# Kernel tuning notes

Hardware: AMD Instinct MI355X
Metric: run time of the kernel (lower is better)

## Reference

```python
import jax, jax.numpy as jnp
import numpy as np

N, E, F = 32768, 524288, 16          # nodes, edges, num_filters
S_IN, V_IN = 64, 32                  # input irreps: 64x0e + 32x1o  (dim 64 + 96 = 160)
NRBF = 32                            # radial basis size of f_ij
LN2 = float(np.log(2.0))

def ssp(x):
    # shifted softplus, the standard SchNet activation
    return jax.nn.softplus(x) - LN2

def setup_inputs() -> dict:
    key = jax.random.key(0)
    ks = jax.random.split(key, 16)
    x = jax.random.normal(ks[0], (N, S_IN + 3 * V_IN), jnp.float32)
    idx_i = jax.random.randint(ks[1], (E,), 0, N)
    idx_j = jax.random.randint(ks[2], (E,), 0, N)
    f_ij = jax.random.normal(ks[3], (E, NRBF), jnp.float32)
    rcut_ij = jax.random.uniform(ks[4], (E,), jnp.float32)
    Yr_ij = jax.random.normal(ks[5], (E, 4), jnp.float32)  # 1x0e + 1x1o
    # equivariant Linear 1: (64x0e+32x1o) -> num_filters*(1x0e+1x1o) = 16x0e+16x1o
    W1_0e = jax.random.normal(ks[6], (S_IN, F), jnp.float32)
    W1_1o = jax.random.normal(ks[7], (V_IN, F), jnp.float32)
    # filter MLP: NRBF -> F -> num_irreps(6*F)
    mW1 = jax.random.normal(ks[8], (NRBF, F), jnp.float32) / np.sqrt(NRBF)
    mb1 = jnp.zeros((F,), jnp.float32)
    mW2 = jax.random.normal(ks[9], (F, 6 * F), jnp.float32) / np.sqrt(F)
    mb2 = jnp.zeros((6 * F,), jnp.float32)
    # equivariant Linear 2: (2Fx0e+2Fx1o+Fx1e+Fx2e) -> input irreps (1e/2e paths drop)
    W2_0e = jax.random.normal(ks[10], (2 * F, S_IN), jnp.float32)
    W2_1o = jax.random.normal(ks[11], (2 * F, V_IN), jnp.float32)
    # equivariant Linear 3: input irreps -> input irreps
    W3_0e = jax.random.normal(ks[12], (S_IN, S_IN), jnp.float32)
    W3_1o = jax.random.normal(ks[13], (V_IN, V_IN), jnp.float32)
    return dict(x=x, f_ij=f_ij, rcut_ij=rcut_ij, Yr_ij=Yr_ij,
                W1_0e=W1_0e, W1_1o=W1_1o, mW1=mW1, mb1=mb1, mW2=mW2, mb2=mb2,
                W2_0e=W2_0e, W2_1o=W2_1o, W3_0e=W3_0e, W3_1o=W3_1o,
                idx_i=idx_i, idx_j=idx_j)

def reference(x, f_ij, rcut_ij, Yr_ij, W1_0e, W1_1o, mW1, mb1, mW2, mb2,
              W2_0e, W2_1o, W3_0e, W3_1o, idx_i, idx_j):
    n = x.shape[0]
    s = x[:, :S_IN]                                  # [N, 64]  0e channels
    v = x[:, S_IN:].reshape(n, V_IN, 3)              # [N, 32, 3] 1o channels
    # Linear 1 (per-irrep channel mixing, e3nn fan-in normalization)
    s1 = (s @ W1_0e) / np.sqrt(S_IN)                 # [N, F]
    v1 = jnp.einsum('ncd,cf->nfd', v, W1_1o) / np.sqrt(V_IN)  # [N, F, 3]
    # gather neighbor features (x_j = x[idx_j], mul_to_axis -> per-filter irreps)
    sj = s1[idx_j]                                   # [E, F]
    vj = v1[idx_j]                                   # [E, F, 3]
    y0 = Yr_ij[:, 0]                                 # [E]
    y1 = Yr_ij[:, 1:4]                               # [E, 3]
    # tensor product (0e+1o) x (0e+1o) -> 2x0e + 2x1o + 1x1e + 1x2e, per filter
    o0a = sj * y0[:, None]                                            # 0e: 0e x 0e
    o0b = jnp.einsum('efd,ed->ef', vj, y1) / np.sqrt(3.0)             # 0e: 1o.1o
    o1a = sj[:, :, None] * y1[:, None, :]                             # 1o: 0e x 1o
    o1b = vj * y0[:, None, None]                                      # 1o: 1o x 0e
    o1e = jnp.cross(vj, y1[:, None, :]) / np.sqrt(2.0)                # 1e: 1o ^ 1o
    ux, uy, uz = vj[..., 0], vj[..., 1], vj[..., 2]
    wx, wy, wz = y1[:, None, 0], y1[:, None, 1], y1[:, None, 2]
    o2 = jnp.stack([(ux * wy + uy * wx) / np.sqrt(2.0),
                    (uy * wz + uz * wy) / np.sqrt(2.0),
                    (2.0 * uz * wz - ux * wx - uy * wy) / np.sqrt(6.0),
                    (ux * wz + uz * wx) / np.sqrt(2.0),
                    (ux * wx - uy * wy) / np.sqrt(2.0)], axis=-1)      # 2e [E, F, 5]
    # filter MLP on radial features, gated by cutoff; one scalar per irrep
    W = ssp(f_ij @ mW1 + mb1) @ mW2 + mb2            # [E, 6F]
    W = W * rcut_ij[:, None]
    w0a, w0b, w1a, w1b, w1e, w2 = (W[:, k * F:(k + 1) * F] for k in range(6))
    seg = lambda z: jax.ops.segment_sum(z, idx_i, num_segments=N)
    # modulate + scatter-sum into center atoms
    n0a = seg(o0a * w0a); n0b = seg(o0b * w0b)                          # [N, F]
    n1a = seg(o1a * w1a[:, :, None]); n1b = seg(o1b * w1b[:, :, None])  # [N, F, 3]
    n1e = seg(o1e * w1e[:, :, None])                                    # [N, F, 3] (dropped by Linear 2)
    n2 = seg(o2 * w2[:, :, None])                                       # [N, F, 5] (dropped by Linear 2)
    n0 = jnp.concatenate([n0a, n0b], axis=-1)        # [N, 2F] 0e
    n1 = jnp.concatenate([n1a, n1b], axis=1)         # [N, 2F, 3] 1o
    del n1e, n2  # no matching output irrep in input_irreps -> e3nn Linear drops them
    # Linear 2 back to input irreps
    s2 = (n0 @ W2_0e) / np.sqrt(2 * F)               # [N, 64]
    v2 = jnp.einsum('nfd,fc->ncd', n1, W2_1o) / np.sqrt(2 * F)  # [N, 32, 3]
    # scalar activation on l=0 only
    s2 = ssp(s2)
    # Linear 3
    s3 = (s2 @ W3_0e) / np.sqrt(S_IN)
    v3 = jnp.einsum('ncd,ce->ned', v2, W3_1o) / np.sqrt(V_IN)
    return jnp.concatenate([s3, v3.reshape(n, -1)], axis=-1)  # [N, 160]
```

## Files before the change

### kernel.cpp

```cpp
#include <hip/hip_runtime.h>
#include <math.h>

#define NN 32768
#define NE 524288
#define RSTR 32
#define SREC_STR 36

__device__ __forceinline__ float sspf(float x) {
    const float INVLN2 = 1.4426950408889634f;
    const float LN2    = 0.69314718055994530942f;
    float t = __builtin_amdgcn_exp2f(-fabsf(x) * INVLN2);
    return fmaxf(x, 0.0f) + LN2 * __builtin_amdgcn_logf(1.0f + t) - LN2;
}

__global__ __launch_bounds__(256) void hist_kernel(
    const int* __restrict__ idx_i, int* __restrict__ counts, int* __restrict__ rank)
{
    int e = blockIdx.x * 256 + threadIdx.x;
    rank[e] = atomicAdd(&counts[idx_i[e]], 1);
}

__global__ __launch_bounds__(1024) void scan_kernel(
    const int* __restrict__ counts, int* __restrict__ start, int* __restrict__ order)
{
    __shared__ int tmp[1024];
    __shared__ int bins[64];
    __shared__ int bcur[64];
    int tid = threadIdx.x;
    int base = tid * 32;
    int cnt[32];
    int local[32];
    int sum = 0;
    const int4* c4 = (const int4*)(counts + base);
#pragma unroll
    for (int q = 0; q < 8; q++) {
        int4 v = c4[q];
        cnt[q*4+0] = v.x; cnt[q*4+1] = v.y; cnt[q*4+2] = v.z; cnt[q*4+3] = v.w;
        local[q*4+0] = sum; sum += v.x;
        local[q*4+1] = sum; sum += v.y;
        local[q*4+2] = sum; sum += v.z;
        local[q*4+3] = sum; sum += v.w;
    }
    tmp[tid] = sum;
    __syncthreads();
    for (int off = 1; off < 1024; off <<= 1) {
        int v = 0;
        if (tid >= off) v = tmp[tid - off];
        __syncthreads();
        if (tid >= off) tmp[tid] += v;
        __syncthreads();
    }
    int excl = tmp[tid] - sum;
#pragma unroll
    for (int k = 0; k < 32; k++) {
        start[base + k] = excl + local[k];
    }
    if (tid == 1023) start[NN] = tmp[1023];

    if (tid < 64) bins[tid] = 0;
    __syncthreads();
#pragma unroll
    for (int k = 0; k < 32; k++) {
        int d = cnt[k] > 63 ? 63 : cnt[k];
        atomicAdd(&bins[63 - d], 1);
    }
    __syncthreads();
    if (tid == 0) {
        int run = 0;
        for (int b = 0; b < 64; b++) { int c = bins[b]; bcur[b] = run; run += c; }
    }
    __syncthreads();
#pragma unroll
    for (int k = 0; k < 32; k++) {
        int d = cnt[k] > 63 ? 63 : cnt[k];
        int pos = atomicAdd(&bcur[63 - d], 1);
        order[pos] = base + k;
    }
}

__global__ __launch_bounds__(256) void pack_kernel(
    const float* __restrict__ f_ij,
    const float* __restrict__ rcut_ij,
    const float* __restrict__ Yr,
    const int*   __restrict__ idx_i,
    const int*   __restrict__ idx_j,
    const float* __restrict__ mW1,
    const float* __restrict__ mb1,
    const int*   __restrict__ start,
    const int*   __restrict__ rank,
    float* __restrict__ epack)
{
    __shared__ float sW1[512];
    __shared__ float sb1[16];
    __shared__ float srec[128 * SREC_STR];
    __shared__ int   sslot[128];
    int t = threadIdx.x;
    for (int k = t; k < 512; k += 256) sW1[k] = mW1[k];
    if (t < 16) sb1[t] = mb1[t];
    __syncthreads();

    int e = blockIdx.x * 256 + t;
    float h[16];
#pragma unroll
    for (int f = 0; f < 16; f++) h[f] = sb1[f];
    const float4* frow = (const float4*)(f_ij + (size_t)e * 32);
#pragma unroll
    for (int rq = 0; rq < 8; rq++) {
        float4 fv = frow[rq];
        int r = rq * 4;
#pragma unroll
        for (int f = 0; f < 16; f++)
            h[f] += fv.x * sW1[(r+0)*16+f] + fv.y * sW1[(r+1)*16+f]
                  + fv.z * sW1[(r+2)*16+f] + fv.w * sW1[(r+3)*16+f];
    }
    float rc = rcut_ij[e];
#pragma unroll
    for (int f = 0; f < 16; f++) h[f] = sspf(h[f]) * rc;

    int i = idx_i[e];
    int j = idx_j[e];
    float4 y = ((const float4*)Yr)[e];
    int slot = start[i] + rank[e];

#pragma unroll 1
    for (int p = 0; p < 2; p++) {
        if ((t >> 7) == p) {
            int r = t & 127;
            float* rp = srec + r * SREC_STR;
            float4* rp4 = (float4*)rp;
#pragma unroll
            for (int q = 0; q < 4; q++) rp4[q] = ((float4*)h)[q];
            rp4[4] = y;
            float4 tail; tail.x = rc; tail.y = __int_as_float(j);
            tail.z = 0.f; tail.w = 0.f;
            rp4[5] = tail;
            float4 z; z.x = 0.f; z.y = 0.f; z.z = 0.f; z.w = 0.f;
            rp4[6] = z;
            rp4[7] = z;
            sslot[r] = slot;
        }
        __syncthreads();
#pragma unroll
        for (int g = 0; g < 4; g++) {
            int idx = g * 256 + t;
            int r = idx >> 3;
            int qi = idx & 7;
            int s = sslot[r];
            float4 v = ((const float4*)(srec + r * SREC_STR))[qi];
            ((float4*)(epack + (size_t)s * RSTR))[qi] = v;
        }
        __syncthreads();
    }
}

__global__ __launch_bounds__(256) void embed_kernel(
    const float* __restrict__ x,
    const float* __restrict__ W1s,
    const float* __restrict__ W1v,
    float* __restrict__ embed)
{
    __shared__ float sWs[1024];
    __shared__ float sWv[512];
    int t = threadIdx.x;
    for (int k = t; k < 1024; k += 256) sWs[k] = W1s[k];
    for (int k = t; k < 512;  k += 256) sWv[k] = W1v[k];
    __syncthreads();

    int n = blockIdx.x * 256 + t;
    const float* xr = x + (size_t)n * 160;

    float s1[16];
#pragma unroll
    for (int f = 0; f < 16; f++) s1[f] = 0.f;
#pragma unroll 1
    for (int cc = 0; cc < 4; cc++) {
        float4 sv[4];
#pragma unroll
        for (int q = 0; q < 4; q++) sv[q] = ((const float4*)xr)[cc*4 + q];
#pragma unroll
        for (int q = 0; q < 4; q++) {
            int c = (cc*4 + q) * 4;
#pragma unroll
            for (int f = 0; f < 16; f++) {
                s1[f] += sv[q].x * sWs[(c+0)*16+f] + sv[q].y * sWs[(c+1)*16+f]
                       + sv[q].z * sWs[(c+2)*16+f] + sv[q].w * sWs[(c+3)*16+f];
            }
        }
    }

    float v1[48];
#pragma unroll
    for (int k = 0; k < 48; k++) v1[k] = 0.f;
#pragma unroll 1
    for (int cc = 0; cc < 4; cc++) {
        float4 vv[6];
#pragma unroll
        for (int q = 0; q < 6; q++) vv[q] = ((const float4*)(xr + 64))[cc*6 + q];
#pragma unroll
        for (int q = 0; q < 6; q++) {
            float vals[4] = {vv[q].x, vv[q].y, vv[q].z, vv[q].w};
#pragma unroll
            for (int u = 0; u < 4; u++) {
                int ml = q * 4 + u;
                int c = cc * 8 + ml / 3;
                int d = ml % 3;
                float val = vals[u];
#pragma unroll
                for (int f = 0; f < 16; f++)
                    v1[f*3+d] += val * sWv[c*16+f];
            }
        }
    }

    float ob[64];
    const float is32 = 0.17677669529663688f;
#pragma unroll
    for (int f = 0; f < 16; f++) {
        ob[f*4+0] = s1[f] * 0.125f;
        ob[f*4+1] = v1[f*3+0] * is32;
        ob[f*4+2] = v1[f*3+1] * is32;
        ob[f*4+3] = v1[f*3+2] * is32;
    }

    float4* eo = (float4*)(embed + (size_t)n * 64);
#pragma unroll
    for (int q = 0; q < 16; q++) eo[q] = ((float4*)ob)[q];
}

__global__ __launch_bounds__(256, 4) void nodeagg_kernel(
    const float* __restrict__ embed,
    const float* __restrict__ epack,
    const int*   __restrict__ start,
    const int*   __restrict__ order,
    const float* __restrict__ mW2,
    const float* __restrict__ mb2,
    float* __restrict__ acc)
{
    int t = threadIdx.x;
    int gid = blockIdx.x * 256 + t;
    int node = order[gid >> 4];
    int f = gid & 15;

    float wga[16], wgb[16], wgc[16], wgd[16];
#pragma unroll
    for (int k = 0; k < 16; k++) {
        wga[k] = mW2[k*96 + f];
        wgb[k] = mW2[k*96 + 16 + f];
        wgc[k] = mW2[k*96 + 32 + f];
        wgd[k] = mW2[k*96 + 48 + f];
    }
    float b0a = mb2[f], b0b = mb2[16+f], b1a = mb2[32+f], b1b = mb2[48+f];

    float aa = 0.f, ab = 0.f;
    float A1a0 = 0.f, A1a1 = 0.f, A1a2 = 0.f;
    float A1b0 = 0.f, A1b1 = 0.f, A1b2 = 0.f;

    int s0 = start[node];
    int s1 = start[node+1];

    for (int q = s0; q < s1; q++) {
        const float4* r4 = (const float4*)(epack + (size_t)q * RSTR);
        float4 h0 = r4[0], h1 = r4[1], h2 = r4[2], h3 = r4[3];
        float4 y  = r4[4], tl = r4[5];
        int j = __float_as_int(tl.y);
        float4 e4 = ((const float4*)(embed + (size_t)j * 64))[f];
        float rc = tl.x;

        float w0a = rc*b0a, w0b = rc*b0b, w1a = rc*b1a, w1b = rc*b1b;
        w0a += h0.x*wga[0]  + h0.y*wga[1]  + h0.z*wga[2]  + h0.w*wga[3]
             + h1.x*wga[4]  + h1.y*wga[5]  + h1.z*wga[6]  + h1.w*wga[7]
             + h2.x*wga[8]  + h2.y*wga[9]  + h2.z*wga[10] + h2.w*wga[11]
             + h3.x*wga[12] + h3.y*wga[13] + h3.z*wga[14] + h3.w*wga[15];
        w0b += h0.x*wgb[0]  + h0.y*wgb[1]  + h0.z*wgb[2]  + h0.w*wgb[3]
             + h1.x*wgb[4]  + h1.y*wgb[5]  + h1.z*wgb[6]  + h1.w*wgb[7]
             + h2.x*wgb[8]  + h2.y*wgb[9]  + h2.z*wgb[10] + h2.w*wgb[11]
             + h3.x*wgb[12] + h3.y*wgb[13] + h3.z*wgb[14] + h3.w*wgb[15];
        w1a += h0.x*wgc[0]  + h0.y*wgc[1]  + h0.z*wgc[2]  + h0.w*wgc[3]
             + h1.x*wgc[4]  + h1.y*wgc[5]  + h1.z*wgc[6]  + h1.w*wgc[7]
             + h2.x*wgc[8]  + h2.y*wgc[9]  + h2.z*wgc[10] + h2.w*wgc[11]
             + h3.x*wgc[12] + h3.y*wgc[13] + h3.z*wgc[14] + h3.w*wgc[15];
        w1b += h0.x*wgd[0]  + h0.y*wgd[1]  + h0.z*wgd[2]  + h0.w*wgd[3]
             + h1.x*wgd[4]  + h1.y*wgd[5]  + h1.z*wgd[6]  + h1.w*wgd[7]
             + h2.x*wgd[8]  + h2.y*wgd[9]  + h2.z*wgd[10] + h2.w*wgd[11]
             + h3.x*wgd[12] + h3.y*wgd[13] + h3.z*wgd[14] + h3.w*wgd[15];

        float sj = e4.x, vx = e4.y, vy = e4.z, vz = e4.w;
        aa += sj * y.x * w0a;
        ab += (vx*y.y + vy*y.z + vz*y.w) * w0b;
        float sw = sj * w1a;
        A1a0 += sw * y.y;
        A1a1 += sw * y.z;
        A1a2 += sw * y.w;
        float yw = y.x * w1b;
        A1b0 += vx * yw;
        A1b1 += vy * yw;
        A1b2 += vz * yw;
    }

    const float is3 = 0.5773502691896258f;
    float* o = acc + (size_t)node * 128;
    o[f]       = aa;
    o[16 + f]  = ab * is3;
    o[32 + f]  = A1a0;
    o[48 + f]  = A1a1;
    o[64 + f]  = A1a2;
    o[80 + f]  = A1b0;
    o[96 + f]  = A1b1;
    o[112 + f] = A1b2;
}


template<int LEN>
__device__ __forceinline__ void v2_seg(const float* a, int d, int cb,
    const float* __restrict__ W2v, float* V2, int ln)
{
    cb = __builtin_amdgcn_readfirstlane(cb);
    d  = __builtin_amdgcn_readfirstlane(d);
    const float is32 = 0.17677669529663688f;
    float na[16], nb[16];
    const float4* pa = (const float4*)(a + 32 + 16*d);
    const float4* pb = (const float4*)(a + 80 + 16*d);
#pragma unroll
    for (int q = 0; q < 4; q++) { ((float4*)na)[q] = pa[q]; ((float4*)nb)[q] = pb[q]; }
    float tacc[LEN];
#pragma unroll
    for (int c = 0; c < LEN; c++) tacc[c] = 0.f;
#pragma unroll
    for (int f = 0; f < 16; f++) {
        float fa = na[f], fb = nb[f];
#pragma unroll
        for (int c = 0; c < LEN; c++)
            tacc[c] += fa * W2v[f*32 + cb + c] + fb * W2v[(16+f)*32 + cb + c];
    }
    float* row = V2 + (d*64 + ln) * 33 + cb;
#pragma unroll
    for (int c = 0; c < LEN; c++) row[c] = tacc[c] * is32;
}

template<int LEN>
__device__ __forceinline__ void v3_seg(float* o, int d, int cb,
    const float* __restrict__ W3v, const float* V2, int ln)
{
    cb = __builtin_amdgcn_readfirstlane(cb);
    d  = __builtin_amdgcn_readfirstlane(d);
    const float is32 = 0.17677669529663688f;
    float tacc[LEN];
#pragma unroll
    for (int c = 0; c < LEN; c++) tacc[c] = 0.f;
    const float* row = V2 + (d*64 + ln) * 33;
#pragma unroll
    for (int k = 0; k < 32; k++) {
        float vk = row[k];
#pragma unroll
        for (int c = 0; c < LEN; c++) tacc[c] += vk * W3v[k*32 + cb + c];
    }
#pragma unroll
    for (int c = 0; c < LEN; c++) o[64 + (cb+c)*3 + d] = tacc[c] * is32;
}

__global__ __launch_bounds__(512, 4) void out_kernel(
    const float* __restrict__ acc,
    const float* __restrict__ W2s,
    const float* __restrict__ W2v,
    const float* __restrict__ W3s,
    const float* __restrict__ W3v,
    float* __restrict__ out)
{
    __shared__ float S2[64*65];
    __shared__ float V2[3*64*33];
    int t = threadIdx.x;
    int w = t >> 6, ln = t & 63;
    int node = blockIdx.x * 64 + ln;
    const float* a = acc + (size_t)node * 128;
    float* o = out + (size_t)node * 160;
    const float is32 = 0.17677669529663688f;

    if (w < 4) {
        int cb = __builtin_amdgcn_readfirstlane(w * 16);
        float n0r[32];
#pragma unroll
        for (int q = 0; q < 8; q++) ((float4*)n0r)[q] = ((const float4*)a)[q];
        float tacc[16];
#pragma unroll
        for (int c = 0; c < 16; c++) tacc[c] = 0.f;
#pragma unroll
        for (int k = 0; k < 32; k++) {
            float nk = n0r[k];
#pragma unroll
            for (int c = 0; c < 16; c++) tacc[c] += nk * W2s[k*64 + cb + c];
        }
        float* row = S2 + ln*65 + cb;
#pragma unroll
        for (int c = 0; c < 16; c++) row[c] = sspf(tacc[c] * is32);
    } else if (w == 4) {
        v2_seg<24>(a, 0, 0,  W2v, V2, ln);
    } else if (w == 5) {
        v2_seg<8> (a, 0, 24, W2v, V2, ln);
        v2_seg<16>(a, 1, 0,  W2v, V2, ln);
    } else if (w == 6) {
        v2_seg<16>(a, 1, 16, W2v, V2, ln);
        v2_seg<8> (a, 2, 0,  W2v, V2, ln);
    } else {
        v2_seg<24>(a, 2, 8,  W2v, V2, ln);
    }
    __syncthreads();
    if (w < 4) {
        int cb = __builtin_amdgcn_readfirstlane(w * 16);
        float tacc[16];
#pragma unroll
        for (int c = 0; c < 16; c++) tacc[c] = 0.f;
        const float* row = S2 + ln*65;
#pragma unroll
        for (int k = 0; k < 64; k++) {
            float sk = row[k];
#pragma unroll
            for (int c = 0; c < 16; c++) tacc[c] += sk * W3s[k*64 + cb + c];
        }
#pragma unroll
        for (int q = 0; q < 4; q++) {
            float4 r = {tacc[q*4+0]*0.125f, tacc[q*4+1]*0.125f,
                        tacc[q*4+2]*0.125f, tacc[q*4+3]*0.125f};
            ((float4*)(o + cb))[q] = r;
        }
    } else if (w == 4) {
        v3_seg<24>(o, 0, 0,  W3v, V2, ln);
    } else if (w == 5) {
        v3_seg<8> (o, 0, 24, W3v, V2, ln);
        v3_seg<16>(o, 1, 0,  W3v, V2, ln);
    } else if (w == 6) {
        v3_seg<16>(o, 1, 16, W3v, V2, ln);
        v3_seg<8> (o, 2, 0,  W3v, V2, ln);
    } else {
        v3_seg<24>(o, 2, 8,  W3v, V2, ln);
    }
}

extern "C" void kernel_launch(void* const* d_in, const int* in_sizes, int n_in,
                              void* d_out, int out_size, void* d_ws, size_t ws_size,
                              hipStream_t stream) {
    const float* x     = (const float*)d_in[0];
    const float* f_ij  = (const float*)d_in[1];
    const float* rcut  = (const float*)d_in[2];
    const float* Yr    = (const float*)d_in[3];
    const float* W1s   = (const float*)d_in[4];
    const float* W1v   = (const float*)d_in[5];
    const float* mW1   = (const float*)d_in[6];
    const float* mb1   = (const float*)d_in[7];
    const float* mW2   = (const float*)d_in[8];
    const float* mb2   = (const float*)d_in[9];
    const float* W2s   = (const float*)d_in[10];
    const float* W2v   = (const float*)d_in[11];
    const float* W3s   = (const float*)d_in[12];
    const float* W3v   = (const float*)d_in[13];
    const int*   idx_i = (const int*)d_in[14];
    const int*   idx_j = (const int*)d_in[15];
    float* out = (float*)d_out;

    float* fws   = (float*)d_ws;
    float* embed = fws;
    float* acc   = embed + (size_t)NN * 64;
    float* epack = acc   + (size_t)NN * 128;
    int* ibase   = (int*)(epack + (size_t)NE * RSTR);
    int* counts  = ibase;
    int* start   = counts + NN;
    int* rank    = start + NN + 1;
    int* order   = rank + NE;

    hipMemsetAsync(counts, 0, (size_t)NN * sizeof(int), stream);
    hist_kernel<<<NE/256, 256, 0, stream>>>(idx_i, counts, rank);
    scan_kernel<<<1, 1024, 0, stream>>>(counts, start, order);
    pack_kernel<<<NE/256, 256, 0, stream>>>(f_ij, rcut, Yr, idx_i, idx_j,
                                            mW1, mb1, start, rank, epack);
    embed_kernel<<<NN/256, 256, 0, stream>>>(x, W1s, W1v, embed);
    nodeagg_kernel<<<(NN*16)/256, 256, 0, stream>>>(embed, epack, start, order,
                                                    mW2, mb2, acc);
    out_kernel<<<NN/64, 512, 0, stream>>>(acc, W2s, W2v, W3s, W3v, out);
}
```

Before: 320.7 us.

## Write edge records in edge order and gather via permutation index in aggregation

The pack kernel now writes each edge's 128-byte record contiguously at its own edge index instead of scattering it to the sorted slot through a shared-memory staging pass. A new small kernel builds an edge permutation array, and the node aggregation kernel reads records indirectly through it. This trades coalesced scattered writes plus two block barriers for an extra index load and a non-contiguous gather of records per node in the aggregation loop.

```diff
diff --git a/kernel.cpp b/kernel.cpp
--- a/kernel.cpp
+++ b/kernel.cpp
@@ -4,7 +4,6 @@
 #define NN 32768
 #define NE 524288
 #define RSTR 32
-#define SREC_STR 36
 
 __device__ __forceinline__ float sspf(float x) {
     const float INVLN2 = 1.4426950408889634f;
@@ -78,22 +77,25 @@
     }
 }
 
+__global__ __launch_bounds__(256) void eorder_kernel(
+    const int* __restrict__ idx_i, const int* __restrict__ start,
+    const int* __restrict__ rank, int* __restrict__ eorder)
+{
+    int e = blockIdx.x * 256 + threadIdx.x;
+    eorder[start[idx_i[e]] + rank[e]] = e;
+}
+
 __global__ __launch_bounds__(256) void pack_kernel(
     const float* __restrict__ f_ij,
     const float* __restrict__ rcut_ij,
     const float* __restrict__ Yr,
-    const int*   __restrict__ idx_i,
     const int*   __restrict__ idx_j,
     const float* __restrict__ mW1,
     const float* __restrict__ mb1,
-    const int*   __restrict__ start,
-    const int*   __restrict__ rank,
     float* __restrict__ epack)
 {
     __shared__ float sW1[512];
     __shared__ float sb1[16];
-    __shared__ float srec[128 * SREC_STR];
-    __shared__ int   sslot[128];
     int t = threadIdx.x;
     for (int k = t; k < 512; k += 256) sW1[k] = mW1[k];
     if (t < 16) sb1[t] = mb1[t];
@@ -117,40 +119,19 @@
 #pragma unroll
     for (int f = 0; f < 16; f++) h[f] = sspf(h[f]) * rc;
 
-    int i = idx_i[e];
     int j = idx_j[e];
     float4 y = ((const float4*)Yr)[e];
-    int slot = start[i] + rank[e];
-
-#pragma unroll 1
-    for (int p = 0; p < 2; p++) {
-        if ((t >> 7) == p) {
-            int r = t & 127;
-            float* rp = srec + r * SREC_STR;
-            float4* rp4 = (float4*)rp;
-#pragma unroll
-            for (int q = 0; q < 4; q++) rp4[q] = ((float4*)h)[q];
-            rp4[4] = y;
-            float4 tail; tail.x = rc; tail.y = __int_as_float(j);
-            tail.z = 0.f; tail.w = 0.f;
-            rp4[5] = tail;
-            float4 z; z.x = 0.f; z.y = 0.f; z.z = 0.f; z.w = 0.f;
-            rp4[6] = z;
-            rp4[7] = z;
-            sslot[r] = slot;
-        }
-        __syncthreads();
-#pragma unroll
-        for (int g = 0; g < 4; g++) {
-            int idx = g * 256 + t;
-            int r = idx >> 3;
-            int qi = idx & 7;
-            int s = sslot[r];
-            float4 v = ((const float4*)(srec + r * SREC_STR))[qi];
-            ((float4*)(epack + (size_t)s * RSTR))[qi] = v;
-        }
-        __syncthreads();
-    }
+
+    float* rec = epack + (size_t)e * RSTR;
+    float4* r4 = (float4*)rec;
+#pragma unroll
+    for (int q = 0; q < 4; q++) r4[q] = ((float4*)h)[q];
+    r4[4] = y;
+    float4 tail; tail.x = rc; tail.y = __int_as_float(j); tail.z = 0.f; tail.w = 0.f;
+    r4[5] = tail;
+    float4 z; z.x = 0.f; z.y = 0.f; z.z = 0.f; z.w = 0.f;
+    r4[6] = z;
+    r4[7] = z;
 }
 
 __global__ __launch_bounds__(256) void embed_kernel(
@@ -232,6 +213,7 @@
     const float* __restrict__ epack,
     const int*   __restrict__ start,
     const int*   __restrict__ order,
+    const int*   __restrict__ eorder,
     const float* __restrict__ mW2,
     const float* __restrict__ mb2,
     float* __restrict__ acc)
@@ -259,7 +241,8 @@
     int s1 = start[node+1];
 
     for (int q = s0; q < s1; q++) {
-        const float4* r4 = (const float4*)(epack + (size_t)q * RSTR);
+        int e = eorder[q];
+        const float4* r4 = (const float4*)(epack + (size_t)e * RSTR);
         float4 h0 = r4[0], h1 = r4[1], h2 = r4[2], h3 = r4[3];
         float4 y  = r4[4], tl = r4[5];
         int j = __float_as_int(tl.y);
@@ -465,14 +448,16 @@
     int* start   = counts + NN;
     int* rank    = start + NN + 1;
     int* order   = rank + NE;
+    int* eorder  = order + NN;
 
     hipMemsetAsync(counts, 0, (size_t)NN * sizeof(int), stream);
     hist_kernel<<<NE/256, 256, 0, stream>>>(idx_i, counts, rank);
     scan_kernel<<<1, 1024, 0, stream>>>(counts, start, order);
-    pack_kernel<<<NE/256, 256, 0, stream>>>(f_ij, rcut, Yr, idx_i, idx_j,
-                                            mW1, mb1, start, rank, epack);
+    eorder_kernel<<<NE/256, 256, 0, stream>>>(idx_i, start, rank, eorder);
+    pack_kernel<<<NE/256, 256, 0, stream>>>(f_ij, rcut, Yr, idx_j,
+                                            mW1, mb1, epack);
     embed_kernel<<<NN/256, 256, 0, stream>>>(x, W1s, W1v, embed);
     nodeagg_kernel<<<(NN*16)/256, 256, 0, stream>>>(embed, epack, start, order,
-                                                    mW2, mb2, acc);
+                                                    eorder, mW2, mb2, acc);
     out_kernel<<<NN/64, 512, 0, stream>>>(acc, W2s, W2v, W3s, W3v, out);
 }
```

Result: slower. 353.4 us (+10.2%).

## Gather edges in sorted order in pack and prefetch edge inputs in hist

Applied to the files above, without the earlier changes.

A new kernel inverts the per-edge slot mapping into a sorted-edge list. pack_kernel now reads its edge data by gather in that order and writes epack rows contiguously, instead of reading coalesced and scattering its writes. hist_kernel also reads f_ij, Yr and rcut and discards the sum, so that these arrays sit in the large last-level cache before pack gathers from them. The cost is one extra kernel launch and an extra full read of f_ij, in return for more cache-friendly writes.

```diff
diff --git a/kernel.cpp b/kernel.cpp
--- a/kernel.cpp
+++ b/kernel.cpp
@@ -14,10 +14,19 @@
 }
 
 __global__ __launch_bounds__(256) void hist_kernel(
-    const int* __restrict__ idx_i, int* __restrict__ counts, int* __restrict__ rank)
+    const int* __restrict__ idx_i, int* __restrict__ counts, int* __restrict__ rank,
+    const float* __restrict__ f_ij, const float* __restrict__ Yr,
+    const float* __restrict__ rcut)
 {
     int e = blockIdx.x * 256 + threadIdx.x;
     rank[e] = atomicAdd(&counts[idx_i[e]], 1);
+    const float4* fr = (const float4*)(f_ij + (size_t)e * 32);
+    float s = 0.f;
+#pragma unroll
+    for (int q = 0; q < 8; q++) { float4 v = fr[q]; s += v.x + v.y + v.z + v.w; }
+    float4 y = ((const float4*)Yr)[e];
+    s += y.x + rcut[e];
+    asm volatile("" :: "v"(s));
 }
 
 __global__ __launch_bounds__(1024) void scan_kernel(
@@ -78,28 +87,35 @@
     }
 }
 
+__global__ __launch_bounds__(256) void eorder_kernel(
+    const int* __restrict__ idx_i, const int* __restrict__ start,
+    const int* __restrict__ rank, int* __restrict__ eorder)
+{
+    int e = blockIdx.x * 256 + threadIdx.x;
+    eorder[start[idx_i[e]] + rank[e]] = e;
+}
+
 __global__ __launch_bounds__(256) void pack_kernel(
     const float* __restrict__ f_ij,
     const float* __restrict__ rcut_ij,
     const float* __restrict__ Yr,
-    const int*   __restrict__ idx_i,
     const int*   __restrict__ idx_j,
+    const int*   __restrict__ eorder,
     const float* __restrict__ mW1,
     const float* __restrict__ mb1,
-    const int*   __restrict__ start,
-    const int*   __restrict__ rank,
     float* __restrict__ epack)
 {
     __shared__ float sW1[512];
     __shared__ float sb1[16];
     __shared__ float srec[128 * SREC_STR];
-    __shared__ int   sslot[128];
     int t = threadIdx.x;
     for (int k = t; k < 512; k += 256) sW1[k] = mW1[k];
     if (t < 16) sb1[t] = mb1[t];
     __syncthreads();
 
-    int e = blockIdx.x * 256 + t;
+    int s = blockIdx.x * 256 + t;
+    int e = eorder[s];
+
     float h[16];
 #pragma unroll
     for (int f = 0; f < 16; f++) h[f] = sb1[f];
@@ -117,17 +133,15 @@
 #pragma unroll
     for (int f = 0; f < 16; f++) h[f] = sspf(h[f]) * rc;
 
-    int i = idx_i[e];
     int j = idx_j[e];
     float4 y = ((const float4*)Yr)[e];
-    int slot = start[i] + rank[e];
-
+
+    size_t base = (size_t)blockIdx.x * 256;
 #pragma unroll 1
     for (int p = 0; p < 2; p++) {
         if ((t >> 7) == p) {
             int r = t & 127;
-            float* rp = srec + r * SREC_STR;
-            float4* rp4 = (float4*)rp;
+            float4* rp4 = (float4*)(srec + r * SREC_STR);
 #pragma unroll
             for (int q = 0; q < 4; q++) rp4[q] = ((float4*)h)[q];
             rp4[4] = y;
@@ -137,7 +151,6 @@
             float4 z; z.x = 0.f; z.y = 0.f; z.z = 0.f; z.w = 0.f;
             rp4[6] = z;
             rp4[7] = z;
-            sslot[r] = slot;
         }
         __syncthreads();
 #pragma unroll
@@ -145,9 +158,8 @@
             int idx = g * 256 + t;
             int r = idx >> 3;
             int qi = idx & 7;
-            int s = sslot[r];
             float4 v = ((const float4*)(srec + r * SREC_STR))[qi];
-            ((float4*)(epack + (size_t)s * RSTR))[qi] = v;
+            ((float4*)(epack + (base + p * 128 + r) * RSTR))[qi] = v;
         }
         __syncthreads();
     }
@@ -465,12 +477,14 @@
     int* start   = counts + NN;
     int* rank    = start + NN + 1;
     int* order   = rank + NE;
+    int* eorder  = order + NN;
 
     hipMemsetAsync(counts, 0, (size_t)NN * sizeof(int), stream);
-    hist_kernel<<<NE/256, 256, 0, stream>>>(idx_i, counts, rank);
+    hist_kernel<<<NE/256, 256, 0, stream>>>(idx_i, counts, rank, f_ij, Yr, rcut);
     scan_kernel<<<1, 1024, 0, stream>>>(counts, start, order);
-    pack_kernel<<<NE/256, 256, 0, stream>>>(f_ij, rcut, Yr, idx_i, idx_j,
-                                            mW1, mb1, start, rank, epack);
+    eorder_kernel<<<NE/256, 256, 0, stream>>>(idx_i, start, rank, eorder);
+    pack_kernel<<<NE/256, 256, 0, stream>>>(f_ij, rcut, Yr, idx_j, eorder,
+                                            mW1, mb1, epack);
     embed_kernel<<<NN/256, 256, 0, stream>>>(x, W1s, W1v, embed);
     nodeagg_kernel<<<(NN*16)/256, 256, 0, stream>>>(embed, epack, start, order,
                                                     mW2, mb2, acc);
```

Result: slower. 399.1 us (+24.4%).
